# Kernel optimization log

Measured on AMD Instinct MI355X. Metric: run time of the kernel, lower is better.

Reference implementation:

```python
import jax, jax.numpy as jnp
import numpy as np

EPS = 1e-5
NUM_HEADS = 6


def _dwconv_bn(x5, W, g, b, m, v, stride):
    # x5: [B, C, H, W, D]; depthwise conv3d (groups=C), kernel 3, pad 1, then eval BatchNorm3d,
    # then rearrange 'b c h w d -> b (h w d) c'
    C = x5.shape[1]
    y = jax.lax.conv_general_dilated(
        x5, W, window_strides=(stride, stride, stride), padding=[(1, 1)] * 3,
        feature_group_count=C, dimension_numbers=('NCDHW', 'OIDHW', 'NCDHW'))
    inv = g / jnp.sqrt(v + EPS)
    y = y * inv[None, :, None, None, None] + (b - m * inv)[None, :, None, None, None]
    B, C2, H, Wd, D = y.shape
    return y.transpose(0, 2, 3, 4, 1).reshape(B, H * Wd * D, C2)


def setup_inputs() -> dict:
    key = jax.random.key(0)
    ks = jax.random.split(key, 24)
    B, T, C = 8, 4096, 384
    hh = ww = dd = 16
    s = 0.02
    inp = {
        'x': jax.random.normal(ks[0], (B, T, C), jnp.float32),
        'conv_q_w': jax.random.normal(ks[1], (C, 1, 3, 3, 3), jnp.float32) * 0.1,
        'conv_k_w': jax.random.normal(ks[2], (C, 1, 3, 3, 3), jnp.float32) * 0.1,
        'conv_v_w': jax.random.normal(ks[3], (C, 1, 3, 3, 3), jnp.float32) * 0.1,
        'bn_q_g': jax.random.uniform(ks[4], (C,), jnp.float32, 0.5, 1.5),
        'bn_q_b': jax.random.normal(ks[5], (C,), jnp.float32) * 0.1,
        'bn_q_m': jax.random.normal(ks[6], (C,), jnp.float32) * 0.1,
        'bn_q_v': jax.random.uniform(ks[7], (C,), jnp.float32, 0.5, 1.5),
        'bn_k_g': jax.random.uniform(ks[8], (C,), jnp.float32, 0.5, 1.5),
        'bn_k_b': jax.random.normal(ks[9], (C,), jnp.float32) * 0.1,
        'bn_k_m': jax.random.normal(ks[10], (C,), jnp.float32) * 0.1,
        'bn_k_v': jax.random.uniform(ks[11], (C,), jnp.float32, 0.5, 1.5),
        'bn_v_g': jax.random.uniform(ks[12], (C,), jnp.float32, 0.5, 1.5),
        'bn_v_b': jax.random.normal(ks[13], (C,), jnp.float32) * 0.1,
        'bn_v_m': jax.random.normal(ks[14], (C,), jnp.float32) * 0.1,
        'bn_v_v': jax.random.uniform(ks[15], (C,), jnp.float32, 0.5, 1.5),
        'wq': jax.random.normal(ks[16], (C, C), jnp.float32) * s,
        'wk': jax.random.normal(ks[17], (C, C), jnp.float32) * s,
        'wv': jax.random.normal(ks[18], (C, C), jnp.float32) * s,
        'proj_w': jax.random.normal(ks[19], (C, C), jnp.float32) * s,
        'proj_b': jax.random.normal(ks[20], (C,), jnp.float32) * s,
        'h': hh, 'w': ww, 'd': dd,
    }
    return inp


def reference(x, conv_q_w, conv_k_w, conv_v_w,
              bn_q_g, bn_q_b, bn_q_m, bn_q_v,
              bn_k_g, bn_k_b, bn_k_m, bn_k_v,
              bn_v_g, bn_v_b, bn_v_m, bn_v_v,
              wq, wk, wv, proj_w, proj_b, h, w, d):
    B, T, C = x.shape
    H = NUM_HEADS
    Dh = C // H
    scale = C ** (-0.5)  # dim_out ** -0.5
    x5 = x.reshape(B, h, w, d, C).transpose(0, 4, 1, 2, 3)  # b (h w d) c -> b c h w d
    q = _dwconv_bn(x5, conv_q_w, bn_q_g, bn_q_b, bn_q_m, bn_q_v, 1)   # [B, T, C]
    k = _dwconv_bn(x5, conv_k_w, bn_k_g, bn_k_b, bn_k_m, bn_k_v, 2)   # [B, Tkv, C]
    v = _dwconv_bn(x5, conv_v_w, bn_v_g, bn_v_b, bn_v_m, bn_v_v, 2)   # [B, Tkv, C]

    def to_heads(t, W):  # Linear (no bias) then 'b t (h d) -> b h t d'
        z = t @ W.T
        return z.reshape(B, -1, H, Dh).transpose(0, 2, 1, 3)

    q = to_heads(q, wq)
    k = to_heads(k, wk)
    v = to_heads(v, wv)
    attn = jax.nn.softmax(jnp.einsum('bhld,bhtd->bhlt', q, k) * scale, axis=-1)
    o = jnp.einsum('bhlt,bhtd->bhld', attn, v)
    o = o.transpose(0, 2, 1, 3).reshape(B, -1, C)  # b h t d -> b t (h d)
    return o @ proj_w.T + proj_b
```

## Files before the change

kernel.cpp:

```cpp
#include <hip/hip_runtime.h>
#include <hip/hip_bf16.h>
#include <stdint.h>


typedef _Float16 f16;
typedef _Float16 f16x8 __attribute__((ext_vector_type(8)));
typedef float f32x4 __attribute__((ext_vector_type(4)));
typedef float f32x16 __attribute__((ext_vector_type(16)));
typedef uint32_t u32;
typedef uint32_t u32x4 __attribute__((ext_vector_type(4)));

#define NC 384
#define MFMA16(A_,B_,C_) __builtin_amdgcn_mfma_f32_16x16x32_f16((A_),(B_),(C_),0,0,0)
#define MFMA32(A_,B_,C_) __builtin_amdgcn_mfma_f32_32x32x16_f16((A_),(B_),(C_),0,0,0)

__device__ __forceinline__ void gll16(const void* g, void* l) {
  __builtin_amdgcn_global_load_lds(
      (__attribute__((address_space(1))) void*)g,
      (__attribute__((address_space(3))) void*)l, 16, 0, 0);
}

__device__ __forceinline__ u32 pkf16(float lo, float hi) {
  return __builtin_bit_cast(u32, __builtin_amdgcn_cvt_pkrtz(lo, hi));
}

__global__ __launch_bounds__(256) void cvt_w(
    const float* __restrict__ s0, const float* __restrict__ s1,
    const float* __restrict__ s2, const float* __restrict__ s3,
    f16* __restrict__ d0, f16* __restrict__ d1,
    f16* __restrict__ d2, f16* __restrict__ d3, int n, float scq)
{
  int i = blockIdx.x * 256 + threadIdx.x;
  if (i < n) {
    d0[i] = (f16)(s0[i] * scq);
    d1[i] = (f16)s1[i]; d2[i] = (f16)s2[i]; d3[i] = (f16)s3[i];
  }
}

__global__ __launch_bounds__(384) void cvt_wt(
    const float* __restrict__ wq, const float* __restrict__ wk, const float* __restrict__ wv,
    const float* __restrict__ bqg, const float* __restrict__ bqb,
    const float* __restrict__ bqm, const float* __restrict__ bqv,
    const float* __restrict__ bkg, const float* __restrict__ bkb,
    const float* __restrict__ bkm, const float* __restrict__ bkv,
    const float* __restrict__ bvg, const float* __restrict__ bvb,
    const float* __restrict__ bvm, const float* __restrict__ bvv,
    float* __restrict__ qT, float* __restrict__ kT, float* __restrict__ vT,
    float* __restrict__ betq, float* __restrict__ betk, float* __restrict__ betv)
{
  const int c = threadIdx.x;
  const int t = blockIdx.x;
  const float invq = bqg[c] * rsqrtf(bqv[c] + 1e-5f);
  const float invk = bkg[c] * rsqrtf(bkv[c] + 1e-5f);
  const float invv = bvg[c] * rsqrtf(bvv[c] + 1e-5f);
  qT[t * 384 + c] = wq[c * 27 + t] * invq;
  kT[t * 384 + c] = wk[c * 27 + t] * invk;
  vT[t * 384 + c] = wv[c * 27 + t] * invv;
  if (t == 0) {
    betq[c] = bqb[c] - bqm[c] * invq;
    betk[c] = bkb[c] - bkm[c] * invk;
    betv[c] = bvb[c] - bvm[c] * invv;
  }
}

__global__ __launch_bounds__(128) void conv_fused(
    const float* __restrict__ x,
    const float* __restrict__ wqT, const float* __restrict__ wkT, const float* __restrict__ wvT,
    const float* __restrict__ betq_, const float* __restrict__ betk_,
    const float* __restrict__ betv_,
    f16* __restrict__ qout, f16* __restrict__ kout, f16* __restrict__ vout)
{
  const int tile = blockIdx.x / 3, cthird = blockIdx.x % 3;
  const int c = cthird * 128 + threadIdx.x;
  const int th = tile >> 3, tw = tile & 7;
  const int b = blockIdx.y;
  const int z0 = blockIdx.z * 4;
  const int h0 = th * 2, w0 = tw * 2;

  float wqr[27], wkr[27], wvr[27];
#pragma unroll
  for (int t = 0; t < 27; ++t) {
    wqr[t] = wqT[t * 384 + c];
    wkr[t] = wkT[t * 384 + c];
    wvr[t] = wvT[t * 384 + c];
  }
  const float betq = betq_[c], betk = betk_[c], betv = betv_[c];

  bool hok[4], wok[4];
#pragma unroll
  for (int a = 0; a < 4; ++a) {
    hok[a] = (unsigned)(h0 - 1 + a) < 16u;
    wok[a] = (unsigned)(w0 - 1 + a) < 16u;
  }
  const float* xb = x + (size_t)b * 4096 * NC + c;

  float win[3][4][4];
  auto ldplane = [&](int s, int iz) {
    const bool zok = (unsigned)iz < 16u;
#pragma unroll
    for (int a = 0; a < 4; ++a)
#pragma unroll
      for (int e = 0; e < 4; ++e) {
        float v = 0.f;
        if (zok && hok[a] && wok[e])
          v = xb[(size_t)((h0 - 1 + a) * 256 + (w0 - 1 + e) * 16 + iz) * NC];
        win[s][a][e] = v;
      }
  };
  ldplane(0, z0 - 1);
  ldplane(1, z0);

#pragma unroll
  for (int zr = 0; zr < 4; ++zr) {
    const int z = z0 + zr;
    ldplane((zr + 2) % 3, z + 1);
    float aq00 = 0.f, aq01 = 0.f, aq10 = 0.f, aq11 = 0.f;
    float ak = 0.f, av = 0.f;
#pragma unroll
    for (int p = 0; p < 3; ++p) {
      const int s = (zr + p) % 3;
#pragma unroll
      for (int a = 0; a < 3; ++a)
#pragma unroll
        for (int e = 0; e < 3; ++e) {
          const float w00 = win[s][a][e],     w01 = win[s][a][e + 1];
          const float w10 = win[s][a + 1][e], w11 = win[s][a + 1][e + 1];
          const float cq = wqr[a * 9 + e * 3 + p];
          aq00 += w00 * cq; aq01 += w01 * cq;
          aq10 += w10 * cq; aq11 += w11 * cq;
          if ((zr & 1) == 0) {
            ak += w00 * wkr[a * 9 + e * 3 + p];
            av += w00 * wvr[a * 9 + e * 3 + p];
          }
        }
    }
    const size_t qb = (size_t)b * 4096;
    qout[(qb + (h0 + 0) * 256 + (w0 + 0) * 16 + z) * NC + c] = (f16)(aq00 + betq);
    qout[(qb + (h0 + 0) * 256 + (w0 + 1) * 16 + z) * NC + c] = (f16)(aq01 + betq);
    qout[(qb + (h0 + 1) * 256 + (w0 + 0) * 16 + z) * NC + c] = (f16)(aq10 + betq);
    qout[(qb + (h0 + 1) * 256 + (w0 + 1) * 16 + z) * NC + c] = (f16)(aq11 + betq);
    if ((zr & 1) == 0) {
      const size_t t = (size_t)b * 512 + tile * 8 + (z >> 1);
      kout[t * NC + c] = (f16)(ak + betk);
      vout[t * NC + c] = (f16)(av + betv);
    }
  }
}

template<int MODE>
__global__ __launch_bounds__(256) void gemm_bt(
    const f16* __restrict__ A, const f16* __restrict__ Bw,
    void* __restrict__ Cout, const float* __restrict__ bias)
{
  __shared__ f16 As[128 * 64];
  __shared__ f16 Bs[128 * 64];
  const int tid = threadIdx.x;
  const int w = tid >> 6, lane = tid & 63;
  const int g = lane >> 4, q = lane & 15;
  const int wr = w >> 1, wc = w & 1;
  const size_t brow = (size_t)blockIdx.y * 128;
  const int bcol = blockIdx.x * 128;
  const int srow = lane >> 3;
  const int sbb  = (lane & 7) ^ (srow & 7);
  f32x4 acc[4][4] = {};
  for (int kt = 0; kt < 6; ++kt) {
    const int k0 = kt * 64;
#pragma unroll
    for (int j = 0; j < 4; ++j) {
      const int s = w * 4 + j;
      gll16(A  + (brow + (size_t)(s * 8 + srow)) * NC + k0 + sbb * 8, (char*)As + s * 1024);
      gll16(Bw + (size_t)(bcol + s * 8 + srow) * NC + k0 + sbb * 8, (char*)Bs + s * 1024);
    }
    __syncthreads();
#pragma unroll
    for (int ks = 0; ks < 2; ++ks) {
      f16x8 af[4], bfr[4];
      const int bb = ((g + 4 * ks) ^ (q & 7)) * 16;
#pragma unroll
      for (int m = 0; m < 4; ++m) {
        af[m]  = *(const f16x8*)((const char*)As + (wr * 64 + m * 16 + q) * 128 + bb);
        bfr[m] = *(const f16x8*)((const char*)Bs + (wc * 64 + m * 16 + q) * 128 + bb);
      }
#pragma unroll
      for (int m = 0; m < 4; ++m)
#pragma unroll
        for (int n = 0; n < 4; ++n)
          acc[m][n] = MFMA16(af[m], bfr[n], acc[m][n]);
    }
    __syncthreads();
  }
  float bvals[4];
  if (MODE == 2) {
#pragma unroll
    for (int n = 0; n < 4; ++n) bvals[n] = bias[bcol + wc * 64 + n * 16 + q];
  }
#pragma unroll
  for (int m = 0; m < 4; ++m) {
#pragma unroll
    for (int n = 0; n < 4; ++n) {
#pragma unroll
      for (int r = 0; r < 4; ++r) {
        const size_t row = brow + wr * 64 + m * 16 + 4 * g + r;
        const int col = bcol + wc * 64 + n * 16 + q;
        const float v = acc[m][n][r];
        if (MODE == 0) {
          ((f16*)Cout)[row * NC + col] = (f16)v;
        } else if (MODE == 1) {
          const size_t bi = row >> 9, t = row & 511;
          ((f16*)Cout)[(bi * NC + col) * 512 + t] = (f16)v;
        } else {
          ((float*)Cout)[row * NC + col] = v + bvals[n];
        }
      }
    }
  }
}

__global__ __launch_bounds__(256) void attn(
    const f16* __restrict__ Qp, const f16* __restrict__ Kp,
    const f16* __restrict__ Vt, f16* __restrict__ O)
{
  __shared__ f16 Ks[2][64 * 64];
  __shared__ f16 Vs[2][64 * 64];
  const int tid = threadIdx.x;
  const int w = tid >> 6, lane = tid & 63;
  const int c = lane & 31, h = lane >> 5;
  const int qt = blockIdx.x, hh = blockIdx.y, b = blockIdx.z;
  const size_t qrow = (size_t)b * 4096 + qt * 128 + w * 32 + c;

  f16x8 qf[4];
#pragma unroll
  for (int ks = 0; ks < 4; ++ks)
    qf[ks] = *(const f16x8*)(Qp + qrow * NC + hh * 64 + ks * 16 + 8 * h);

  f32x16 oa0 = {}, oa1 = {};
  float l_run = 0.f;

  const int r0 = tid >> 3, k0b = tid & 7;
  const int r1 = (tid + 256) >> 3, k1b = tid & 7;
  const f16* ks0 = Kp + ((size_t)b * 512 + r0) * NC + hh * 64 + ((k0b ^ (r0 & 7)) * 8);
  const f16* ks1 = Kp + ((size_t)b * 512 + r1) * NC + hh * 64 + ((k1b ^ (r1 & 7)) * 8);
  const f16* vs0 = Vt + ((size_t)b * NC + hh * 64 + r0) * 512 + ((k0b ^ (r0 & 7)) * 8);
  const f16* vs1 = Vt + ((size_t)b * NC + hh * 64 + r1) * 512 + ((k1b ^ (r1 & 7)) * 8);
  gll16(ks0, (char*)&Ks[0][0] + tid * 16);
  gll16(ks1, (char*)&Ks[0][0] + (tid + 256) * 16);
  gll16(vs0, (char*)&Vs[0][0] + tid * 16);
  gll16(vs1, (char*)&Vs[0][0] + (tid + 256) * 16);

  int buf = 0;
  for (int ch = 0; ch < 8; ++ch) {
    __syncthreads();
    if (ch < 7) {
      gll16(ks0 + (size_t)(ch + 1) * 64 * NC, (char*)&Ks[buf ^ 1][0] + tid * 16);
      gll16(ks1 + (size_t)(ch + 1) * 64 * NC, (char*)&Ks[buf ^ 1][0] + (tid + 256) * 16);
      gll16(vs0 + (ch + 1) * 64, (char*)&Vs[buf ^ 1][0] + tid * 16);
      gll16(vs1 + (ch + 1) * 64, (char*)&Vs[buf ^ 1][0] + (tid + 256) * 16);
    }
    const char* kb = (const char*)&Ks[buf][0];
    const char* vb = (const char*)&Vs[buf][0];
#pragma unroll
    for (int half = 0; half < 2; ++half) {
      f32x16 st = {};
#pragma unroll
      for (int ks = 0; ks < 4; ++ks) {
        const int bo = ((2 * ks + h) ^ (c & 7)) * 16;
        const f16x8 kf = *(const f16x8*)(kb + (32 * half + c) * 128 + bo);
        st = MFMA32(kf, qf[ks], st);
      }
      u32 pk[8];
      float ps0 = 0.f, ps1 = 0.f;
#pragma unroll
      for (int t = 0; t < 8; ++t) {
        const float a0 = __builtin_amdgcn_exp2f(st[2 * t]);
        const float a1 = __builtin_amdgcn_exp2f(st[2 * t + 1]);
        ps0 += a0; ps1 += a1;
        pk[t] = pkf16(a0, a1);
      }
      l_run += ps0 + ps1;
#pragma unroll
      for (int ss = 0; ss < 2; ++ss) {
        const int s = half * 2 + ss, tb = ss * 4;
        const u32 xs = h ? pk[tb + 0] : pk[tb + 2];
        const u32 ys = h ? pk[tb + 1] : pk[tb + 3];
        const u32 rx = __shfl_xor(xs, 32);
        const u32 ry = __shfl_xor(ys, 32);
        u32x4 fi;
        fi[0] = h ? rx : pk[tb + 0];
        fi[1] = h ? ry : pk[tb + 1];
        fi[2] = h ? pk[tb + 2] : rx;
        fi[3] = h ? pk[tb + 3] : ry;
        const f16x8 pfrag = __builtin_bit_cast(f16x8, fi);
        const int bo = ((2 * s + h) ^ (c & 7)) * 16;
        const f16x8 v0 = *(const f16x8*)(vb + c * 128 + bo);
        const f16x8 v1 = *(const f16x8*)(vb + (32 + c) * 128 + bo);
        oa0 = MFMA32(v0, pfrag, oa0);
        oa1 = MFMA32(v1, pfrag, oa1);
      }
    }
    buf ^= 1;
  }
  const float ltot = l_run + __shfl_xor(l_run, 32);
  const float linv = 1.0f / ltot;
  f16* orow = O + qrow * NC + hh * 64;
#pragma unroll
  for (int dt = 0; dt < 2; ++dt) {
#pragma unroll
    for (int qd = 0; qd < 4; ++qd) {
      const float v0 = (dt ? oa1[4 * qd + 0] : oa0[4 * qd + 0]) * linv;
      const float v1 = (dt ? oa1[4 * qd + 1] : oa0[4 * qd + 1]) * linv;
      const float v2 = (dt ? oa1[4 * qd + 2] : oa0[4 * qd + 2]) * linv;
      const float v3 = (dt ? oa1[4 * qd + 3] : oa0[4 * qd + 3]) * linv;
      uint2 pr; pr.x = pkf16(v0, v1); pr.y = pkf16(v2, v3);
      *(uint2*)(orow + dt * 32 + 8 * qd + 4 * h) = pr;
    }
  }
}

extern "C" void kernel_launch(void* const* d_in, const int* in_sizes, int n_in,
                              void* d_out, int out_size, void* d_ws, size_t ws_size,
                              hipStream_t stream) {
  const float* x   = (const float*)d_in[0];
  const float* cqw = (const float*)d_in[1];
  const float* ckw = (const float*)d_in[2];
  const float* cvw = (const float*)d_in[3];
  const float* bqg = (const float*)d_in[4],  *bqb = (const float*)d_in[5];
  const float* bqm = (const float*)d_in[6],  *bqv = (const float*)d_in[7];
  const float* bkg = (const float*)d_in[8],  *bkb = (const float*)d_in[9];
  const float* bkm = (const float*)d_in[10], *bkv = (const float*)d_in[11];
  const float* bvg = (const float*)d_in[12], *bvb = (const float*)d_in[13];
  const float* bvm = (const float*)d_in[14], *bvv = (const float*)d_in[15];
  const float* wq = (const float*)d_in[16];
  const float* wk = (const float*)d_in[17];
  const float* wv = (const float*)d_in[18];
  const float* pw = (const float*)d_in[19];
  const float* pb = (const float*)d_in[20];

  f16* q_tok = (f16*)d_out;
  f16* Qp    = (f16*)((char*)d_out + 25165824);

  char* ws = (char*)d_ws;
  f16* wq_h  = (f16*)(ws + 0);
  f16* wk_h  = (f16*)(ws + 294912);
  f16* wv_h  = (f16*)(ws + 589824);
  f16* pw_h  = (f16*)(ws + 884736);
  f16* k_tok = (f16*)(ws + 1179648);
  f16* v_tok = (f16*)(ws + 4325376);
  f16* Kp    = (f16*)(ws + 7471104);
  f16* Vt    = (f16*)(ws + 10616832);
  f16* Oi    = (f16*)(ws + 13762560);
  float* wqT = (float*)(ws + 38928384);
  float* wkT = (float*)(ws + 38969856);
  float* wvT = (float*)(ws + 39011328);
  float* betq = (float*)(ws + 39052800);
  float* betk = (float*)(ws + 39054336);
  float* betv = (float*)(ws + 39055872);

  const float scq = 0.051031036307982884f * 1.4426950408889634f;
  cvt_w<<<dim3(576), dim3(256), 0, stream>>>(wq, wk, wv, pw, wq_h, wk_h, wv_h, pw_h,
                                             147456, scq);
  cvt_wt<<<dim3(27), dim3(384), 0, stream>>>(
      cqw, ckw, cvw,
      bqg, bqb, bqm, bqv, bkg, bkb, bkm, bkv, bvg, bvb, bvm, bvv,
      wqT, wkT, wvT, betq, betk, betv);
  conv_fused<<<dim3(192, 8, 4), dim3(128), 0, stream>>>(
      x, wqT, wkT, wvT, betq, betk, betv, q_tok, k_tok, v_tok);
  gemm_bt<0><<<dim3(3, 256), dim3(256), 0, stream>>>(q_tok, wq_h, Qp, nullptr);
  gemm_bt<0><<<dim3(3, 32),  dim3(256), 0, stream>>>(k_tok, wk_h, Kp, nullptr);
  gemm_bt<1><<<dim3(3, 32),  dim3(256), 0, stream>>>(v_tok, wv_h, Vt, nullptr);
  attn<<<dim3(32, 6, 8), dim3(256), 0, stream>>>(Qp, Kp, Vt, Oi);
  gemm_bt<2><<<dim3(3, 256), dim3(256), 0, stream>>>(Oi, pw_h, d_out, pb);
}
```

Measured before the change: 152.0 us.

## Fuse Q projection GEMM into attention kernel prologue

Removes the separate Q projection GEMM launch and computes the per-head 128x64 Q tile inside the attention kernel with MFMA, staging q_tok and Wq slices through the K/V shared buffers. The goal is to avoid writing and re-reading the full projected Q tensor in global memory and to drop one launch. In exchange, each attention block re-reads the 128x384 q_tok tile for every head, which is six times redundant across heads. It also adds extra LDS (a Qtmp buffer) and syncs, which may lower occupancy.

```diff
diff --git a/kernel.cpp b/kernel.cpp
--- a/kernel.cpp
+++ b/kernel.cpp
@@ -217,36 +217,82 @@
 }
 
 __global__ __launch_bounds__(256) void attn(
-    const f16* __restrict__ Qp, const f16* __restrict__ Kp,
-    const f16* __restrict__ Vt, f16* __restrict__ O)
+    const f16* __restrict__ qtok, const f16* __restrict__ wqh,
+    const f16* __restrict__ Kp, const f16* __restrict__ Vt, f16* __restrict__ O)
 {
   __shared__ f16 Ks[2][64 * 64];
   __shared__ f16 Vs[2][64 * 64];
+  __shared__ f16 Qtmp[128 * 72];
   const int tid = threadIdx.x;
   const int w = tid >> 6, lane = tid & 63;
   const int c = lane & 31, h = lane >> 5;
   const int qt = blockIdx.x, hh = blockIdx.y, b = blockIdx.z;
-  const size_t qrow = (size_t)b * 4096 + qt * 128 + w * 32 + c;
-
+  const size_t qrow0b = (size_t)b * 4096 + qt * 128;
+  const size_t qrow = qrow0b + w * 32 + c;
+
+  const int r0 = tid >> 3, k0b = tid & 7;
+  const int r1 = (tid + 256) >> 3;
+  const f16* ks0 = Kp + ((size_t)b * 512 + r0) * NC + hh * 64 + ((k0b ^ (r0 & 7)) * 8);
+  const f16* ks1 = Kp + ((size_t)b * 512 + r1) * NC + hh * 64 + ((k0b ^ (r1 & 7)) * 8);
+  const f16* vs0 = Vt + ((size_t)b * NC + hh * 64 + r0) * 512 + ((k0b ^ (r0 & 7)) * 8);
+  const f16* vs1 = Vt + ((size_t)b * NC + hh * 64 + r1) * 512 + ((k0b ^ (r1 & 7)) * 8);
+  gll16(vs0, (char*)&Vs[0][0] + tid * 16);
+  gll16(vs1, (char*)&Vs[0][0] + (tid + 256) * 16);
+
+  {
+    char* QsFlat = (char*)&Ks[0][0];
+    char* WqFlat = (char*)&Vs[1][0];
+    const int srow = lane >> 3, sbb = (lane & 7) ^ (srow & 7);
+    f32x16 qa0 = {}, qa1 = {};
+    for (int kt = 0; kt < 6; ++kt) {
+#pragma unroll
+      for (int j = 0; j < 4; ++j) {
+        const int s = w * 4 + j;
+        gll16(qtok + (qrow0b + (size_t)(s * 8 + srow)) * NC + kt * 64 + sbb * 8,
+              QsFlat + s * 1024);
+      }
+#pragma unroll
+      for (int j = 0; j < 2; ++j) {
+        const int i = tid + j * 256;
+        const int row = i >> 3, blk = i & 7;
+        gll16(wqh + (size_t)(hh * 64 + row) * NC + kt * 64 + ((blk ^ (row & 7)) * 8),
+              WqFlat + i * 16);
+      }
+      __syncthreads();
+#pragma unroll
+      for (int ks = 0; ks < 4; ++ks) {
+        const int bo = ((2 * ks + h) ^ (c & 7)) * 16;
+        const f16x8 bq = *(const f16x8*)(QsFlat + (w * 32 + c) * 128 + bo);
+        const f16x8 a0 = *(const f16x8*)(WqFlat + c * 128 + bo);
+        const f16x8 a1 = *(const f16x8*)(WqFlat + (32 + c) * 128 + bo);
+        qa0 = MFMA32(a0, bq, qa0);
+        qa1 = MFMA32(a1, bq, qa1);
+      }
+      __syncthreads();
+    }
+#pragma unroll
+    for (int t = 0; t < 2; ++t) {
+#pragma unroll
+      for (int g4 = 0; g4 < 4; ++g4) {
+        const float q0 = t ? qa1[4 * g4 + 0] : qa0[4 * g4 + 0];
+        const float q1 = t ? qa1[4 * g4 + 1] : qa0[4 * g4 + 1];
+        const float q2 = t ? qa1[4 * g4 + 2] : qa0[4 * g4 + 2];
+        const float q3 = t ? qa1[4 * g4 + 3] : qa0[4 * g4 + 3];
+        uint2 pr; pr.x = pkf16(q0, q1); pr.y = pkf16(q2, q3);
+        *(uint2*)((char*)Qtmp + ((w * 32 + c) * 72 + t * 32 + 8 * g4 + 4 * h) * 2) = pr;
+      }
+    }
+    __syncthreads();
+  }
   f16x8 qf[4];
 #pragma unroll
   for (int ks = 0; ks < 4; ++ks)
-    qf[ks] = *(const f16x8*)(Qp + qrow * NC + hh * 64 + ks * 16 + 8 * h);
+    qf[ks] = *(const f16x8*)((const char*)Qtmp + ((w * 32 + c) * 72 + ks * 16 + 8 * h) * 2);
+  gll16(ks0, (char*)&Ks[0][0] + tid * 16);
+  gll16(ks1, (char*)&Ks[0][0] + (tid + 256) * 16);
 
   f32x16 oa0 = {}, oa1 = {};
   float l_run = 0.f;
-
-  const int r0 = tid >> 3, k0b = tid & 7;
-  const int r1 = (tid + 256) >> 3, k1b = tid & 7;
-  const f16* ks0 = Kp + ((size_t)b * 512 + r0) * NC + hh * 64 + ((k0b ^ (r0 & 7)) * 8);
-  const f16* ks1 = Kp + ((size_t)b * 512 + r1) * NC + hh * 64 + ((k1b ^ (r1 & 7)) * 8);
-  const f16* vs0 = Vt + ((size_t)b * NC + hh * 64 + r0) * 512 + ((k0b ^ (r0 & 7)) * 8);
-  const f16* vs1 = Vt + ((size_t)b * NC + hh * 64 + r1) * 512 + ((k1b ^ (r1 & 7)) * 8);
-  gll16(ks0, (char*)&Ks[0][0] + tid * 16);
-  gll16(ks1, (char*)&Ks[0][0] + (tid + 256) * 16);
-  gll16(vs0, (char*)&Vs[0][0] + tid * 16);
-  gll16(vs1, (char*)&Vs[0][0] + (tid + 256) * 16);
-
   int buf = 0;
   for (int ch = 0; ch < 8; ++ch) {
     __syncthreads();
@@ -336,7 +382,6 @@
   const float* pb = (const float*)d_in[20];
 
   f16* q_tok = (f16*)d_out;
-  f16* Qp    = (f16*)((char*)d_out + 25165824);
 
   char* ws = (char*)d_ws;
   f16* wq_h  = (f16*)(ws + 0);
@@ -364,9 +409,8 @@
       wqT, wkT, wvT, betq, betk, betv);
   conv_fused<<<dim3(192, 8, 4), dim3(128), 0, stream>>>(
       x, wqT, wkT, wvT, betq, betk, betv, q_tok, k_tok, v_tok);
-  gemm_bt<0><<<dim3(3, 256), dim3(256), 0, stream>>>(q_tok, wq_h, Qp, nullptr);
   gemm_bt<0><<<dim3(3, 32),  dim3(256), 0, stream>>>(k_tok, wk_h, Kp, nullptr);
   gemm_bt<1><<<dim3(3, 32),  dim3(256), 0, stream>>>(v_tok, wv_h, Vt, nullptr);
-  attn<<<dim3(32, 6, 8), dim3(256), 0, stream>>>(Qp, Kp, Vt, Oi);
+  attn<<<dim3(32, 6, 8), dim3(256), 0, stream>>>(q_tok, wq_h, Kp, Vt, Oi);
   gemm_bt<2><<<dim3(3, 256), dim3(256), 0, stream>>>(Oi, pw_h, d_out, pb);
 }
```

Result: faster. 141.1 us (-7.1%).
